# Optimization experiments

Hardware: AMD Instinct MI355X
Metric: run time of the kernel (lower is better)

## Reference

```python
import jax, jax.numpy as jnp
import numpy as np
import math

IN_C = 512
OUT_C = 512
K = 3
STYLE = 512
EPS = 1e-8
MOD_SCALE = 1.0 / math.sqrt(STYLE)        # EqualLinear scale (lr_mul=1)
CONV_SCALE = 1.0 / math.sqrt(IN_C * K * K)  # ModulatedConv2d scale


def setup_inputs() -> dict:
    key = jax.random.key(0)
    k1, k2, k3, k4 = jax.random.split(key, 4)
    return {
        "x": jax.random.normal(k1, (8, IN_C, 64, 64), dtype=jnp.float32),
        "style": jax.random.normal(k2, (8, STYLE), dtype=jnp.float32),
        "mod_weight": jax.random.normal(k3, (IN_C, STYLE), dtype=jnp.float32),
        "mod_bias": jnp.ones((IN_C,), dtype=jnp.float32),
        "weight": jax.random.normal(k4, (1, OUT_C, IN_C, K, K), dtype=jnp.float32),
    }


def _per_sample_conv(xi, wi):
    # xi: [in_c, H, W], wi: [out_c, in_c, K, K]
    out = jax.lax.conv_general_dilated(
        xi[None], wi, window_strides=(1, 1), padding="SAME",
        dimension_numbers=("NCHW", "OIHW", "NCHW"))
    return out[0]


def reference(x, style, mod_weight, mod_bias, weight):
    # EqualLinear modulation: s = style @ (W*scale)^T + bias  -> [B, in_c]
    s = style @ (mod_weight * MOD_SCALE).T + mod_bias
    # per-sample modulated weight: [B, out_c, in_c, K, K]
    w = CONV_SCALE * weight * s[:, None, :, None, None]
    demod = jax.lax.rsqrt(jnp.sum(w * w, axis=(2, 3, 4), keepdims=True) + EPS)
    w = w * demod
    # grouped conv (groups=batch) == vmap of per-sample conv
    out = jax.vmap(_per_sample_conv)(x, w)  # [B, out_c, H, W]
    return out
```

## Files before the change

### kernel.cpp

```cpp
#include <hip/hip_runtime.h>
#include <hip/hip_bf16.h>

typedef __attribute__((ext_vector_type(8))) short bf16x8;
typedef __attribute__((ext_vector_type(4))) float f32x4;
typedef unsigned int u32;

#define MOD_SCALE 0.04419417382415922f
#define CONV_SCALE 0.014731391274719742f

__device__ __forceinline__ unsigned short f2bf(float f) {
  union { float f; u32 u; } v; v.f = f;
  u32 r = v.u + 0x7fffu + ((v.u >> 16) & 1u);
  return (unsigned short)(r >> 16);
}

__device__ __forceinline__ void gload_lds16(const void* g, void* l) {
  __builtin_amdgcn_global_load_lds(
      (const __attribute__((address_space(1))) u32*)g,
      (__attribute__((address_space(3))) u32*)l, 16, 0, 0);
}

__global__ void k_style(const float* __restrict__ style, const float* __restrict__ mw,
                        const float* __restrict__ mb, float* __restrict__ s) {
  int idx = blockIdx.x * 256 + threadIdx.x;
  int b = idx >> 9, ic = idx & 511;
  const float4* wr = (const float4*)(mw + ic * 512);
  const float4* sr = (const float4*)(style + b * 512);
  float acc = 0.f;
  #pragma unroll 4
  for (int k = 0; k < 128; ++k) {
    float4 a = wr[k], c = sr[k];
    acc += a.x * c.x + a.y * c.y + a.z * c.z + a.w * c.w;
  }
  s[idx] = acc * MOD_SCALE + mb[ic];
}

__global__ void k_wprep(const float* __restrict__ wsrc, ushort* __restrict__ wb,
                        float* __restrict__ wsq, float* __restrict__ zerobuf) {
  int idx = blockIdx.x * 256 + threadIdx.x;
  if (blockIdx.x == 0 && threadIdx.x < 16) zerobuf[threadIdx.x] = 0.f;
  const float* wp = wsrc + (size_t)idx * 9;
  float sq = 0.f;
  #pragma unroll
  for (int tap = 0; tap < 9; ++tap) {
    float v = wp[tap];
    sq += v * v;
    wb[tap * 262144 + idx] = f2bf(v);
  }
  wsq[idx] = sq;
}

__global__ void k_demod(const float* __restrict__ wsq, const float* __restrict__ s,
                        float* __restrict__ dscale) {
  int idx = blockIdx.x * 256 + threadIdx.x;
  int b = idx >> 9, oc = idx & 511;
  const float4* wq = (const float4*)(wsq + oc * 512);
  const float4* sp = (const float4*)(s + b * 512);
  float acc = 0.f;
  #pragma unroll 4
  for (int k = 0; k < 128; ++k) {
    float4 a = wq[k], c = sp[k];
    acc += a.x * c.x * c.x + a.y * c.y * c.y + a.z * c.z * c.z + a.w * c.w * c.w;
  }
  dscale[idx] = CONV_SCALE * rsqrtf(CONV_SCALE * CONV_SCALE * acc + 1e-8f);
}

__global__ void k_xform(const float* __restrict__ x, const float* __restrict__ s,
                        ushort* __restrict__ xsb) {
  const int y = blockIdx.x, icb = blockIdx.y, b = blockIdx.z;
  const int t = threadIdx.x;
  __shared__ ushort tile[64][67];
  const int px = t & 63, icq = t >> 6;
  #pragma unroll
  for (int i = 0; i < 16; ++i) {
    int ic_l = i * 4 + icq;
    int ic = icb * 64 + ic_l;
    float v = x[(b * 512 + ic) * 4096 + y * 64 + px] * s[b * 512 + ic];
    tile[ic_l][px] = f2bf(v);
  }
  __syncthreads();
  const int kp = t & 31, pq = t >> 5;
  ushort* obase = xsb + ((b * 64 + y) * 64) * 512 + icb * 64 + kp * 2;
  #pragma unroll
  for (int i = 0; i < 8; ++i) {
    int p = i * 8 + pq;
    ushort2 u;
    u.x = tile[kp * 2][p];
    u.y = tile[kp * 2 + 1][p];
    *(ushort2*)(obase + p * 512) = u;
  }
}

__global__ __launch_bounds__(256, 2) void k_conv(
    const ushort* __restrict__ wb, const ushort* __restrict__ xsb,
    const float* __restrict__ dscale, const float* __restrict__ zerobuf,
    float* __restrict__ out) {
  const int yb = blockIdx.x, ocb = blockIdx.y, b = blockIdx.z;
  const int t = threadIdx.x;
  const int wv = t >> 6, l = t & 63;
  const int ln = l & 15, lq = l >> 4;
  const int y0 = yb * 4;

  __shared__ __align__(16) ushort As[9 * 64 * 32];
  __shared__ __align__(16) ushort Bs[6 * 66 * 32];
  __shared__ float dss[64];

  if (t < 64) dss[t] = dscale[b * 512 + ocb * 64 + t];

  f32x4 acc[4][4];
  #pragma unroll
  for (int m = 0; m < 4; ++m)
    #pragma unroll
    for (int n = 0; n < 4; ++n)
      acc[m][n] = f32x4{0.f, 0.f, 0.f, 0.f};

  const int aslot = lq ^ ((ln >> 1) & 3);
  int bslot[3];
  #pragma unroll
  for (int dx = 0; dx < 3; ++dx) bslot[dx] = lq ^ (((ln + dx) >> 1) & 3);

  const int a_ocl = t >> 2, a_q = t & 3;
  const int a_qs = a_q ^ ((a_ocl >> 1) & 3);
  const char* srcA0 = (const char*)(wb + (ocb * 64 + a_ocl) * 512 + a_qs * 8);
  char* ldsA0 = (char*)As + wv * 1024;

  int bvalid[7];
  const char* bsrc_base[7];
  char* bdst[7];
  #pragma unroll
  for (int i = 0; i < 7; ++i) {
    int cid = i * 256 + t;
    int r = cid / 264;
    int rem = cid - r * 264;
    int c = rem >> 2, q = rem & 3;
    int yy = y0 - 1 + r, xx = c - 1;
    int qs = q ^ ((c >> 1) & 3);
    bvalid[i] = (cid < 1584) && ((unsigned)yy < 64u) && ((unsigned)xx < 64u);
    bsrc_base[i] = bvalid[i]
        ? (const char*)(xsb + ((b * 64 + yy) * 64 + xx) * 512 + qs * 8)
        : (const char*)zerobuf;
    bdst[i] = (char*)Bs + (i * 256 + wv * 64) * 16;
  }

  #pragma unroll 1
  for (int icb_i = 0; icb_i < 16; ++icb_i) {
    const int icB = icb_i * 64;
    #pragma unroll
    for (int i = 0; i < 9; ++i)
      gload_lds16(srcA0 + i * 524288 + icB, ldsA0 + i * 4096);
    #pragma unroll
    for (int i = 0; i < 7; ++i) {
      if (i < 6 || t < 48) {
        const char* src = bvalid[i] ? bsrc_base[i] + icB : (const char*)zerobuf;
        gload_lds16(src, bdst[i]);
      }
    }
    __syncthreads();
    #pragma unroll
    for (int dy = 0; dy < 3; ++dy) {
      const int r = wv + dy;
      #pragma unroll
      for (int dx = 0; dx < 3; ++dx) {
        const int tap = dy * 3 + dx;
        bf16x8 af[4], bfr[4];
        #pragma unroll
        for (int m = 0; m < 4; ++m)
          af[m] = *(const bf16x8*)((const char*)As + tap * 4096 + (m * 16 + ln) * 64 + aslot * 16);
        #pragma unroll
        for (int n = 0; n < 4; ++n) {
          int c = n * 16 + ln + dx;
          bfr[n] = *(const bf16x8*)((const char*)Bs + (r * 66 + c) * 64 + bslot[dx] * 16);
        }
        #pragma unroll
        for (int m = 0; m < 4; ++m)
          #pragma unroll
          for (int n = 0; n < 4; ++n)
            acc[m][n] = __builtin_amdgcn_mfma_f32_16x16x32_bf16(af[m], bfr[n], acc[m][n], 0, 0, 0);
      }
    }
    __syncthreads();
  }

  const int y_row = y0 + wv;
  #pragma unroll
  for (int m = 0; m < 4; ++m) {
    #pragma unroll
    for (int r4 = 0; r4 < 4; ++r4) {
      const int oc_l = m * 16 + lq * 4 + r4;
      const float sc = dss[oc_l];
      float* op = out + ((b * 512 + ocb * 64 + oc_l) * 4096 + y_row * 64);
      #pragma unroll
      for (int n = 0; n < 4; ++n)
        op[n * 16 + ln] = acc[m][n][r4] * sc;
    }
  }
}

extern "C" void kernel_launch(void* const* d_in, const int* in_sizes, int n_in,
                              void* d_out, int out_size, void* d_ws, size_t ws_size,
                              hipStream_t stream) {
  const float* x     = (const float*)d_in[0];
  const float* style = (const float*)d_in[1];
  const float* mw    = (const float*)d_in[2];
  const float* mb    = (const float*)d_in[3];
  const float* wsrc  = (const float*)d_in[4];
  float* out = (float*)d_out;

  char* ws = (char*)d_ws;
  float*  zerobuf = (float*)(ws + 0);
  float*  s       = (float*)(ws + 256);
  float*  dscale  = (float*)(ws + 16640);
  float*  wsq     = (float*)(ws + 33024);
  ushort* wb      = (ushort*)(ws + 1081600);
  ushort* xsb     = (ushort*)(ws + 5800192);

  k_style<<<dim3(16), dim3(256), 0, stream>>>(style, mw, mb, s);
  k_wprep<<<dim3(1024), dim3(256), 0, stream>>>(wsrc, wb, wsq, zerobuf);
  k_demod<<<dim3(16), dim3(256), 0, stream>>>(wsq, s, dscale);
  k_xform<<<dim3(64, 8, 8), dim3(256), 0, stream>>>(x, s, xsb);
  k_conv<<<dim3(16, 8, 8), dim3(256), 0, stream>>>(wb, xsb, dscale, zerobuf, out);
}
```

Measured before the change: 194.4 us.

## Double-buffer conv LDS stages with 8-row tiles and vectorize xform transpose

The conv kernel now uses 512-thread blocks covering 8 output rows, with the weight and input tiles double-buffered in dynamic LDS. The next input-channel chunk is prefetched while the current one is computed, which hides global-load latency and halves the number of blocks. The halo overhead per row also drops. The xform kernel packs 8 channels per 16-byte store instead of ushort2 writes. The cost is about 158KB of LDS, which limits the kernel to one block per CU, and there is a risk from lower occupancy.

```diff
diff --git a/kernel.cpp b/kernel.cpp
--- a/kernel.cpp
+++ b/kernel.cpp
@@ -67,31 +67,37 @@
 
 __global__ void k_xform(const float* __restrict__ x, const float* __restrict__ s,
                         ushort* __restrict__ xsb) {
-  const int y = blockIdx.x, icb = blockIdx.y, b = blockIdx.z;
+  const int y = blockIdx.x, b = blockIdx.y, ich = blockIdx.z;
   const int t = threadIdx.x;
-  __shared__ ushort tile[64][67];
-  const int px = t & 63, icq = t >> 6;
-  #pragma unroll
-  for (int i = 0; i < 16; ++i) {
-    int ic_l = i * 4 + icq;
-    int ic = icb * 64 + ic_l;
-    float v = x[(b * 512 + ic) * 4096 + y * 64 + px] * s[b * 512 + ic];
-    tile[ic_l][px] = f2bf(v);
+  __shared__ ushort T[64 * 264];
+  const int px = t & 63, iq = t >> 6;
+  const int icbase = ich * 256;
+  #pragma unroll
+  for (int i = 0; i < 8; ++i) {
+    int ic8 = i * 4 + iq;
+    int ic0 = icbase + ic8 * 8;
+    union { ushort u[8]; uint4 v; } pk;
+    #pragma unroll
+    for (int j = 0; j < 8; ++j) {
+      int ic = ic0 + j;
+      float v = x[(b * 512 + ic) * 4096 + y * 64 + px] * s[b * 512 + ic];
+      pk.u[j] = f2bf(v);
+    }
+    *(uint4*)&T[px * 264 + ic8 * 8] = pk.v;
   }
   __syncthreads();
-  const int kp = t & 31, pq = t >> 5;
-  ushort* obase = xsb + ((b * 64 + y) * 64) * 512 + icb * 64 + kp * 2;
+  const int ch = t & 31;
+  ushort* obase = xsb + ((b * 64 + y) * 64) * 512 + icbase + ch * 8;
   #pragma unroll
   for (int i = 0; i < 8; ++i) {
-    int p = i * 8 + pq;
-    ushort2 u;
-    u.x = tile[kp * 2][p];
-    u.y = tile[kp * 2 + 1][p];
-    *(ushort2*)(obase + p * 512) = u;
-  }
-}
-
-__global__ __launch_bounds__(256, 2) void k_conv(
+    int p = i * 8 + (t >> 5);
+    uint4 v = *(const uint4*)&T[p * 264 + ch * 8];
+    *(uint4*)(obase + p * 512) = v;
+  }
+}
+
+#define BUFB 79104
+__global__ __launch_bounds__(512, 1) void k_conv(
     const ushort* __restrict__ wb, const ushort* __restrict__ xsb,
     const float* __restrict__ dscale, const float* __restrict__ zerobuf,
     float* __restrict__ out) {
@@ -99,11 +105,10 @@
   const int t = threadIdx.x;
   const int wv = t >> 6, l = t & 63;
   const int ln = l & 15, lq = l >> 4;
-  const int y0 = yb * 4;
-
-  __shared__ __align__(16) ushort As[9 * 64 * 32];
-  __shared__ __align__(16) ushort Bs[6 * 66 * 32];
-  __shared__ float dss[64];
+  const int y0 = yb * 8;
+
+  extern __shared__ char smem[];
+  float* dss = (float*)(smem + 2 * BUFB);
 
   if (t < 64) dss[t] = dscale[b * 512 + ocb * 64 + t];
 
@@ -119,58 +124,65 @@
   #pragma unroll
   for (int dx = 0; dx < 3; ++dx) bslot[dx] = lq ^ (((ln + dx) >> 1) & 3);
 
-  const int a_ocl = t >> 2, a_q = t & 3;
-  const int a_qs = a_q ^ ((a_ocl >> 1) & 3);
-  const char* srcA0 = (const char*)(wb + (ocb * 64 + a_ocl) * 512 + a_qs * 8);
-  char* ldsA0 = (char*)As + wv * 1024;
-
-  int bvalid[7];
-  const char* bsrc_base[7];
-  char* bdst[7];
-  #pragma unroll
-  for (int i = 0; i < 7; ++i) {
-    int cid = i * 256 + t;
+  const int a_ocl = (t & 255) >> 2;
+  const int a_qs = (t & 3) ^ ((a_ocl >> 1) & 3);
+  const int a_tb = t >> 8;
+  const char* srcA = (const char*)(wb + (ocb * 64 + a_ocl) * 512 + a_qs * 8);
+  const int a_dstw = wv * 1024;
+
+  int bpart[6];
+  const char* bsrc[6];
+  int bdstc[6];
+  #pragma unroll
+  for (int i = 0; i < 6; ++i) {
+    int cid = i * 512 + t;
     int r = cid / 264;
     int rem = cid - r * 264;
     int c = rem >> 2, q = rem & 3;
     int yy = y0 - 1 + r, xx = c - 1;
     int qs = q ^ ((c >> 1) & 3);
-    bvalid[i] = (cid < 1584) && ((unsigned)yy < 64u) && ((unsigned)xx < 64u);
-    bsrc_base[i] = bvalid[i]
-        ? (const char*)(xsb + ((b * 64 + yy) * 64 + xx) * 512 + qs * 8)
-        : (const char*)zerobuf;
-    bdst[i] = (char*)Bs + (i * 256 + wv * 64) * 16;
-  }
-
-  #pragma unroll 1
-  for (int icb_i = 0; icb_i < 16; ++icb_i) {
-    const int icB = icb_i * 64;
-    #pragma unroll
-    for (int i = 0; i < 9; ++i)
-      gload_lds16(srcA0 + i * 524288 + icB, ldsA0 + i * 4096);
-    #pragma unroll
-    for (int i = 0; i < 7; ++i) {
-      if (i < 6 || t < 48) {
-        const char* src = bvalid[i] ? bsrc_base[i] + icB : (const char*)zerobuf;
-        gload_lds16(src, bdst[i]);
+    bpart[i] = (cid < 2640);
+    int geo_ok = bpart[i] && ((unsigned)yy < 64u) && ((unsigned)xx < 64u);
+    bsrc[i] = geo_ok ? (const char*)(xsb + ((b * 64 + yy) * 64 + xx) * 512 + qs * 8)
+                     : (const char*)nullptr;
+    bdstc[i] = (i * 512 + wv * 64) * 16;
+  }
+
+  auto STAGE = [&](int boff, int icB) {
+    char* Ab = smem + boff;
+    char* Bb = smem + boff + 36864;
+    #pragma unroll
+    for (int i = 0; i < 4; ++i) {
+      int tap = 2 * i + a_tb;
+      gload_lds16(srcA + tap * 524288 + icB, Ab + i * 8192 + a_dstw);
+    }
+    if (t < 256)
+      gload_lds16(srcA + 8 * 524288 + icB, Ab + 4 * 8192 + a_dstw);
+    #pragma unroll
+    for (int i = 0; i < 6; ++i) {
+      if (bpart[i]) {
+        const char* src = bsrc[i] ? bsrc[i] + icB : (const char*)zerobuf;
+        gload_lds16(src, Bb + bdstc[i]);
       }
     }
-    __syncthreads();
+  };
+
+  auto COMPUTE = [&](int boff) {
+    const char* Ab = smem + boff;
+    const char* Bb = smem + boff + 36864;
     #pragma unroll
     for (int dy = 0; dy < 3; ++dy) {
-      const int r = wv + dy;
+      const int row = wv + dy;
       #pragma unroll
       for (int dx = 0; dx < 3; ++dx) {
         const int tap = dy * 3 + dx;
         bf16x8 af[4], bfr[4];
         #pragma unroll
         for (int m = 0; m < 4; ++m)
-          af[m] = *(const bf16x8*)((const char*)As + tap * 4096 + (m * 16 + ln) * 64 + aslot * 16);
+          af[m] = *(const bf16x8*)(Ab + tap * 4096 + (m * 16 + ln) * 64 + aslot * 16);
         #pragma unroll
-        for (int n = 0; n < 4; ++n) {
-          int c = n * 16 + ln + dx;
-          bfr[n] = *(const bf16x8*)((const char*)Bs + (r * 66 + c) * 64 + bslot[dx] * 16);
-        }
+        for (int n = 0; n < 4; ++n)
+          bfr[n] = *(const bf16x8*)(Bb + (row * 66 + n * 16 + ln + dx) * 64 + bslot[dx] * 16);
         #pragma unroll
         for (int m = 0; m < 4; ++m)
           #pragma unroll
@@ -178,6 +190,14 @@
             acc[m][n] = __builtin_amdgcn_mfma_f32_16x16x32_bf16(af[m], bfr[n], acc[m][n], 0, 0, 0);
       }
     }
+  };
+
+  STAGE(0, 0);
+  __syncthreads();
+  #pragma unroll 1
+  for (int it = 0; it < 16; ++it) {
+    if (it < 15) STAGE(((it + 1) & 1) * BUFB, (it + 1) * 64);
+    COMPUTE((it & 1) * BUFB);
     __syncthreads();
   }
 
@@ -214,9 +234,12 @@
   ushort* wb      = (ushort*)(ws + 1081600);
   ushort* xsb     = (ushort*)(ws + 5800192);
 
+  hipFuncSetAttribute(reinterpret_cast<const void*>(k_conv),
+                      hipFuncAttributeMaxDynamicSharedMemorySize, 2 * BUFB + 256);
+
   k_style<<<dim3(16), dim3(256), 0, stream>>>(style, mw, mb, s);
   k_wprep<<<dim3(1024), dim3(256), 0, stream>>>(wsrc, wb, wsq, zerobuf);
   k_demod<<<dim3(16), dim3(256), 0, stream>>>(wsq, s, dscale);
-  k_xform<<<dim3(64, 8, 8), dim3(256), 0, stream>>>(x, s, xsb);
-  k_conv<<<dim3(16, 8, 8), dim3(256), 0, stream>>>(wb, xsb, dscale, zerobuf, out);
-}
+  k_xform<<<dim3(64, 8, 2), dim3(256), 0, stream>>>(x, s, xsb);
+  k_conv<<<dim3(8, 8, 8), dim3(512), 2 * BUFB + 256, stream>>>(wb, xsb, dscale, zerobuf, out);
+}
```

Measured after the change: 190.2 us. 1.02x faster.
